# Optimization experiments

Measured on AMD Instinct MI355X. Metric: run time of the kernel, lower is better.

The kernel has to match this reference:

```python
import jax, jax.numpy as jnp
import numpy as np

BLOCK_SIZE = 32
MODEL_DIM = 64
HEAD_SIZE = 64
WINDOW_SIZE = 8
B = 32768


def _local_causal_mask(T, window):
    # True = masked out. Allowed iff i - window + 1 <= j <= i.
    i = jnp.arange(T)[:, None]
    j = jnp.arange(T)[None, :]
    return (j > i) | (j < i - window + 1)


def setup_inputs() -> dict:
    key = jax.random.key(0)
    kx, kq, kk, kv = jax.random.split(key, 4)
    x = jax.random.normal(kx, (B, BLOCK_SIZE, MODEL_DIM), dtype=jnp.float32)
    # nn.Linear(model_dim, head_size, bias=False): y = x @ W.T, W: [head_size, model_dim].
    # Store as [model_dim, head_size] so y = x @ W.
    s = 1.0 / np.sqrt(MODEL_DIM)
    Wq = jax.random.uniform(kq, (MODEL_DIM, HEAD_SIZE), jnp.float32, -s, s)
    Wk = jax.random.uniform(kk, (MODEL_DIM, HEAD_SIZE), jnp.float32, -s, s)
    Wv = jax.random.uniform(kv, (MODEL_DIM, HEAD_SIZE), jnp.float32, -s, s)
    return {"x": x, "Wq": Wq, "Wk": Wk, "Wv": Wv}


def reference(x, Wq, Wk, Wv):
    B_, T, C = x.shape
    q = x @ Wq  # [B, T, H]
    k = x @ Wk
    v = x @ Wv
    scale = k.shape[-1] ** -0.5
    weight = jnp.einsum("bth,bsh->bts", q, k) * scale  # [B, T, T]
    mask = _local_causal_mask(T, WINDOW_SIZE)
    weight = jnp.where(mask[None, :, :], -jnp.inf, weight)
    attention_weights = jax.nn.softmax(weight, axis=-1)
    # dropout treated as identity (eval mode) for determinism
    output = jnp.einsum("bts,bsh->bth", attention_weights, v)
    return (output, attention_weights)
```

## Files before the change

### kernel.cpp

```cpp
#include <hip/hip_runtime.h>
#include <math.h>

typedef float f32x4 __attribute__((ext_vector_type(4)));
typedef unsigned int u32x4 __attribute__((ext_vector_type(4)));
typedef short bf16x8 __attribute__((ext_vector_type(8)));

__device__ __forceinline__ unsigned f2bf1(float f) {
  unsigned u = __builtin_bit_cast(unsigned, f);
  return (u + 0x7FFFu + ((u >> 16) & 1u)) >> 16;
}
__device__ __forceinline__ unsigned pack2(float a, float b) {
  return f2bf1(a) | (f2bf1(b) << 16);
}

__device__ __forceinline__ f32x4 mfma16(u32x4 a, u32x4 b, f32x4 c) {
  return __builtin_amdgcn_mfma_f32_16x16x32_bf16(
      __builtin_bit_cast(bf16x8, a), __builtin_bit_cast(bf16x8, b), c, 0, 0, 0);
}

template <int NS, int NF, int NKS>
__device__ __forceinline__ void cvt_frags(const f32x4 (&acc)[NS][NF],
                                          u32x4 (&frag)[NF][NKS],
                                          int f, int g) {
  unsigned pk[NS][NF][2];
#pragma unroll
  for (int s = 0; s < NS; ++s)
#pragma unroll
    for (int n = 0; n < NF; ++n) {
      pk[s][n][0] = pack2(acc[s][n][0], acc[s][n][1]);
      pk[s][n][1] = pack2(acc[s][n][2], acc[s][n][3]);
    }
  const bool hi = ((g >> 1) & 1) != 0;
#pragma unroll
  for (int w = 0; w < 4; ++w) {
    const int gp = 2 * (g & 1) + (w >> 1);
    const int idx = (f + (gp << 4)) << 2;
#pragma unroll
    for (int n = 0; n < NF; ++n)
#pragma unroll
      for (int ks = 0; ks < NKS; ++ks) {
        int lo = __builtin_amdgcn_ds_bpermute(idx, (int)pk[2 * ks + 0][n][w & 1]);
        int h2 = __builtin_amdgcn_ds_bpermute(idx, (int)pk[2 * ks + 1][n][w & 1]);
        frag[n][ks][w] = (unsigned)(hi ? h2 : lo);
      }
  }
}

__launch_bounds__(256, 2)
__global__ void lwmh_kernel(const float* __restrict__ x,
                            const float* __restrict__ Wq,
                            const float* __restrict__ Wk,
                            const float* __restrict__ Wv,
                            float* __restrict__ out,
                            float* __restrict__ attw,
                            int nb) {
  const int lane = threadIdx.x & 63;
  const int f = lane & 15;
  const int g = lane >> 4;
  const int wid = blockIdx.x * (blockDim.x >> 6) + (threadIdx.x >> 6);
  const int nwaves = gridDim.x * (blockDim.x >> 6);

  u32x4 wq[4][2], wk[4][2], wv[4][2];
  {
#pragma unroll
    for (int t = 0; t < 4; ++t)
#pragma unroll
      for (int ks = 0; ks < 2; ++ks) {
        const int off = (ks * 32 + g * 8) * 64 + t * 16 + f;
        const float* bq = Wq + off;
        const float* bk = Wk + off;
        const float* bv = Wv + off;
        u32x4 fq, fk, fv;
#pragma unroll
        for (int w = 0; w < 4; ++w) {
          fq[w] = pack2(bq[(2 * w) * 64], bq[(2 * w + 1) * 64]);
          fk[w] = pack2(bk[(2 * w) * 64], bk[(2 * w + 1) * 64]);
          fv[w] = pack2(bv[(2 * w) * 64], bv[(2 * w + 1) * 64]);
        }
        wq[t][ks] = fq;
        wk[t][ks] = fk;
        wv[t][ks] = fv;
      }
  }

  f32x4 xc[2][2][2], xn[2][2][2];

  auto loadX = [&](int b, f32x4 (&xr)[2][2][2]) {
    const float* xb = x + (size_t)b * 2048;
#pragma unroll
    for (int mt = 0; mt < 2; ++mt)
#pragma unroll
      for (int ks = 0; ks < 2; ++ks) {
        const float* p0 = xb + (mt * 16 + f) * 64 + ks * 32 + g * 8;
        xr[mt][ks][0] = *(const f32x4*)p0;
        xr[mt][ks][1] = *(const f32x4*)(p0 + 4);
      }
  };

  int b = wid;
  if (b < nb) loadX(b, xc);

  for (; b < nb; b += nwaves) {
    const int bn = b + nwaves;

    u32x4 xf[2][2];
#pragma unroll
    for (int mt = 0; mt < 2; ++mt)
#pragma unroll
      for (int ks = 0; ks < 2; ++ks) {
        u32x4 fr;
        fr[0] = pack2(xc[mt][ks][0][0], xc[mt][ks][0][1]);
        fr[1] = pack2(xc[mt][ks][0][2], xc[mt][ks][0][3]);
        fr[2] = pack2(xc[mt][ks][1][0], xc[mt][ks][1][1]);
        fr[3] = pack2(xc[mt][ks][1][2], xc[mt][ks][1][3]);
        xf[mt][ks] = fr;
      }

    if (bn < nb) loadX(bn, xn);

    f32x4 qt[4][2];
#pragma unroll
    for (int mh = 0; mh < 4; ++mh)
#pragma unroll
      for (int nt = 0; nt < 2; ++nt) {
        f32x4 a = {0.f, 0.f, 0.f, 0.f};
#pragma unroll
        for (int ks = 0; ks < 2; ++ks) a = mfma16(wq[mh][ks], xf[nt][ks], a);
        qt[mh][nt] = a;
      }
    u32x4 aQ[2][2];
    cvt_frags<4, 2, 2>(qt, aQ, f, g);

    f32x4 kt[4][2];
#pragma unroll
    for (int mh = 0; mh < 4; ++mh)
#pragma unroll
      for (int nt = 0; nt < 2; ++nt) {
        f32x4 a = {0.f, 0.f, 0.f, 0.f};
#pragma unroll
        for (int ks = 0; ks < 2; ++ks) a = mfma16(wk[mh][ks], xf[nt][ks], a);
        kt[mh][nt] = a;
      }
    u32x4 aK[2][2];
    cvt_frags<4, 2, 2>(kt, aK, f, g);

    f32x4 va[2][4];
#pragma unroll
    for (int ms = 0; ms < 2; ++ms)
#pragma unroll
      for (int nh = 0; nh < 4; ++nh) {
        f32x4 a = {0.f, 0.f, 0.f, 0.f};
#pragma unroll
        for (int ks = 0; ks < 2; ++ks) a = mfma16(xf[ms][ks], wv[nh][ks], a);
        va[ms][nh] = a;
      }
    u32x4 bV[4][1];
    cvt_frags<2, 4, 1>(va, bV, f, g);

    f32x4 st[2][2];
#pragma unroll
    for (int ms = 0; ms < 2; ++ms)
#pragma unroll
      for (int nt = 0; nt < 2; ++nt) {
        f32x4 a = {0.f, 0.f, 0.f, 0.f};
#pragma unroll
        for (int ks = 0; ks < 2; ++ks) a = mfma16(aK[ms][ks], aQ[nt][ks], a);
        st[ms][nt] = a;
      }

    float pe[2][2][4];
#pragma unroll
    for (int nt = 0; nt < 2; ++nt) {
      const int t = nt * 16 + f;
      float m = -INFINITY;
#pragma unroll
      for (int ms = 0; ms < 2; ++ms)
#pragma unroll
        for (int r = 0; r < 4; ++r) {
          const int s = ms * 16 + 4 * g + r;
          float v = st[ms][nt][r] * 0.125f;
          v = (t >= s && (t - s) <= 7) ? v : -INFINITY;
          pe[ms][nt][r] = v;
          m = fmaxf(m, v);
        }
      m = fmaxf(m, __shfl_xor(m, 16));
      m = fmaxf(m, __shfl_xor(m, 32));
      float sum = 0.f;
#pragma unroll
      for (int ms = 0; ms < 2; ++ms)
#pragma unroll
        for (int r = 0; r < 4; ++r) {
          const float e = __expf(pe[ms][nt][r] - m);
          pe[ms][nt][r] = e;
          sum += e;
        }
      sum += __shfl_xor(sum, 16);
      sum += __shfl_xor(sum, 32);
      const float inv = 1.0f / sum;
#pragma unroll
      for (int ms = 0; ms < 2; ++ms)
#pragma unroll
        for (int r = 0; r < 4; ++r) pe[ms][nt][r] *= inv;
    }

    {
      float* aw = attw + (size_t)b * 1024;
#pragma unroll
      for (int ms = 0; ms < 2; ++ms)
#pragma unroll
        for (int nt = 0; nt < 2; ++nt)
#pragma unroll
          for (int r = 0; r < 4; ++r)
            aw[(nt * 16 + f) * 32 + ms * 16 + 4 * g + r] = pe[ms][nt][r];
    }

    f32x4 pacc[2][2];
#pragma unroll
    for (int ms = 0; ms < 2; ++ms)
#pragma unroll
      for (int nt = 0; nt < 2; ++nt) {
        f32x4 a;
        a[0] = pe[ms][nt][0];
        a[1] = pe[ms][nt][1];
        a[2] = pe[ms][nt][2];
        a[3] = pe[ms][nt][3];
        pacc[ms][nt] = a;
      }
    u32x4 aP[2][1];
    cvt_frags<2, 2, 1>(pacc, aP, f, g);

    f32x4 o[2][4];
#pragma unroll
    for (int mt = 0; mt < 2; ++mt)
#pragma unroll
      for (int nh = 0; nh < 4; ++nh) {
        f32x4 a = {0.f, 0.f, 0.f, 0.f};
        o[mt][nh] = mfma16(aP[mt][0], bV[nh][0], a);
      }

    {
      float* op = out + (size_t)b * 2048;
#pragma unroll
      for (int mt = 0; mt < 2; ++mt)
#pragma unroll
        for (int nh = 0; nh < 4; ++nh)
#pragma unroll
          for (int r = 0; r < 4; ++r)
            op[(mt * 16 + 4 * g + r) * 64 + nh * 16 + f] = o[mt][nh][r];
    }

    if (bn < nb) {
#pragma unroll
      for (int mt = 0; mt < 2; ++mt)
#pragma unroll
        for (int ks = 0; ks < 2; ++ks) {
          xc[mt][ks][0] = xn[mt][ks][0];
          xc[mt][ks][1] = xn[mt][ks][1];
        }
    }
  }
}

extern "C" void kernel_launch(void* const* d_in, const int* in_sizes, int n_in,
                              void* d_out, int out_size, void* d_ws, size_t ws_size,
                              hipStream_t stream) {
  const float* x = (const float*)d_in[0];
  const float* Wq = (const float*)d_in[1];
  const float* Wk = (const float*)d_in[2];
  const float* Wv = (const float*)d_in[3];
  const int nb = in_sizes[0] / 2048;
  float* out = (float*)d_out;
  float* attw = out + (size_t)nb * 2048;

  const int grid = 1024;
  lwmh_kernel<<<grid, 256, 0, stream>>>(x, Wq, Wk, Wv, out, attw, nb);
}
```

Measured before the change: 146.2 us.

## Fold Wq·WkT into a precomputed matrix and drop softmax max subtraction

Precomputes N = Wq·Wk^T·scale once per wave, so scores become x·(N·x^T). This replaces the separate Q and K projections and their fragment conversions with one projection plus one conversion. Softmax no longer subtracts the row maximum and only exponentiates inside the window. Attention weights are now written with vectorized 16-byte stores, and the next x load is issued earlier. Skipping the max subtraction relies on scores staying small enough not to overflow exp, and the extra bf16 rounding of N changes numerics.

Result: no change. 146.3 us (+0.1%).

```diff
diff --git a/kernel.cpp b/kernel.cpp
--- a/kernel.cpp
+++ b/kernel.cpp
@@ -60,27 +60,53 @@
   const int wid = blockIdx.x * (blockDim.x >> 6) + (threadIdx.x >> 6);
   const int nwaves = gridDim.x * (blockDim.x >> 6);
 
-  u32x4 wq[4][2], wk[4][2], wv[4][2];
-  {
-#pragma unroll
-    for (int t = 0; t < 4; ++t)
-#pragma unroll
-      for (int ks = 0; ks < 2; ++ks) {
-        const int off = (ks * 32 + g * 8) * 64 + t * 16 + f;
-        const float* bq = Wq + off;
-        const float* bk = Wk + off;
-        const float* bv = Wv + off;
-        u32x4 fq, fk, fv;
-#pragma unroll
-        for (int w = 0; w < 4; ++w) {
-          fq[w] = pack2(bq[(2 * w) * 64], bq[(2 * w + 1) * 64]);
-          fk[w] = pack2(bk[(2 * w) * 64], bk[(2 * w + 1) * 64]);
-          fv[w] = pack2(bv[(2 * w) * 64], bv[(2 * w + 1) * 64]);
-        }
-        wq[t][ks] = fq;
-        wk[t][ks] = fk;
-        wv[t][ks] = fv;
-      }
+  u32x4 aWq[4][2], bWkT[4][2];
+#pragma unroll
+  for (int ct = 0; ct < 4; ++ct)
+#pragma unroll
+    for (int hs = 0; hs < 2; ++hs) {
+      const int off = (ct * 16 + f) * 64 + hs * 32 + g * 8;
+      f32x4 ql = *(const f32x4*)(Wq + off);
+      f32x4 qh = *(const f32x4*)(Wq + off + 4);
+      f32x4 kl = *(const f32x4*)(Wk + off);
+      f32x4 kh = *(const f32x4*)(Wk + off + 4);
+      u32x4 fq, fk;
+      fq[0] = pack2(ql[0], ql[1]); fq[1] = pack2(ql[2], ql[3]);
+      fq[2] = pack2(qh[0], qh[1]); fq[3] = pack2(qh[2], qh[3]);
+      fk[0] = pack2(kl[0], kl[1]); fk[1] = pack2(kl[2], kl[3]);
+      fk[2] = pack2(kh[0], kh[1]); fk[3] = pack2(kh[2], kh[3]);
+      aWq[ct][hs] = fq;
+      bWkT[ct][hs] = fk;
+    }
+
+  u32x4 wv[4][2];
+#pragma unroll
+  for (int t = 0; t < 4; ++t)
+#pragma unroll
+    for (int ks = 0; ks < 2; ++ks) {
+      const float* bv = Wv + (ks * 32 + g * 8) * 64 + t * 16 + f;
+      u32x4 fv;
+#pragma unroll
+      for (int w = 0; w < 4; ++w)
+        fv[w] = pack2(bv[(2 * w) * 64], bv[(2 * w + 1) * 64]);
+      wv[t][ks] = fv;
+    }
+
+  u32x4 aN[4][2];
+#pragma unroll
+  for (int nc = 0; nc < 4; ++nc) {
+    f32x4 nacc[4][1];
+#pragma unroll
+    for (int mc = 0; mc < 4; ++mc) {
+      f32x4 a = {0.f, 0.f, 0.f, 0.f};
+#pragma unroll
+      for (int hs = 0; hs < 2; ++hs) a = mfma16(aWq[mc][hs], bWkT[nc][hs], a);
+      nacc[mc][0] = a * 0.125f;
+    }
+    u32x4 tmp[1][2];
+    cvt_frags<4, 1, 2>(nacc, tmp, f, g);
+    aN[nc][0] = tmp[0][0];
+    aN[nc][1] = tmp[0][1];
   }
 
   f32x4 xc[2][2][2], xn[2][2][2];
@@ -102,6 +128,7 @@
 
   for (; b < nb; b += nwaves) {
     const int bn = b + nwaves;
+    if (bn < nb) loadX(bn, xn);
 
     u32x4 xf[2][2];
 #pragma unroll
@@ -116,33 +143,18 @@
         xf[mt][ks] = fr;
       }
 
-    if (bn < nb) loadX(bn, xn);
-
-    f32x4 qt[4][2];
-#pragma unroll
-    for (int mh = 0; mh < 4; ++mh)
+    f32x4 t2[4][2];
+#pragma unroll
+    for (int mc = 0; mc < 4; ++mc)
 #pragma unroll
       for (int nt = 0; nt < 2; ++nt) {
         f32x4 a = {0.f, 0.f, 0.f, 0.f};
 #pragma unroll
-        for (int ks = 0; ks < 2; ++ks) a = mfma16(wq[mh][ks], xf[nt][ks], a);
-        qt[mh][nt] = a;
-      }
-    u32x4 aQ[2][2];
-    cvt_frags<4, 2, 2>(qt, aQ, f, g);
-
-    f32x4 kt[4][2];
-#pragma unroll
-    for (int mh = 0; mh < 4; ++mh)
-#pragma unroll
-      for (int nt = 0; nt < 2; ++nt) {
-        f32x4 a = {0.f, 0.f, 0.f, 0.f};
-#pragma unroll
-        for (int ks = 0; ks < 2; ++ks) a = mfma16(wk[mh][ks], xf[nt][ks], a);
-        kt[mh][nt] = a;
-      }
-    u32x4 aK[2][2];
-    cvt_frags<4, 2, 2>(kt, aK, f, g);
+        for (int ks = 0; ks < 2; ++ks) a = mfma16(aN[mc][ks], xf[nt][ks], a);
+        t2[mc][nt] = a;
+      }
+    u32x4 bT2[2][2];
+    cvt_frags<4, 2, 2>(t2, bT2, f, g);
 
     f32x4 va[2][4];
 #pragma unroll
@@ -164,33 +176,22 @@
       for (int nt = 0; nt < 2; ++nt) {
         f32x4 a = {0.f, 0.f, 0.f, 0.f};
 #pragma unroll
-        for (int ks = 0; ks < 2; ++ks) a = mfma16(aK[ms][ks], aQ[nt][ks], a);
+        for (int ks = 0; ks < 2; ++ks) a = mfma16(xf[ms][ks], bT2[nt][ks], a);
         st[ms][nt] = a;
       }
 
-    float pe[2][2][4];
+    f32x4 pe[2][2];
 #pragma unroll
     for (int nt = 0; nt < 2; ++nt) {
       const int t = nt * 16 + f;
-      float m = -INFINITY;
+      float sum = 0.f;
 #pragma unroll
       for (int ms = 0; ms < 2; ++ms)
 #pragma unroll
         for (int r = 0; r < 4; ++r) {
           const int s = ms * 16 + 4 * g + r;
-          float v = st[ms][nt][r] * 0.125f;
-          v = (t >= s && (t - s) <= 7) ? v : -INFINITY;
-          pe[ms][nt][r] = v;
-          m = fmaxf(m, v);
-        }
-      m = fmaxf(m, __shfl_xor(m, 16));
-      m = fmaxf(m, __shfl_xor(m, 32));
-      float sum = 0.f;
-#pragma unroll
-      for (int ms = 0; ms < 2; ++ms)
-#pragma unroll
-        for (int r = 0; r < 4; ++r) {
-          const float e = __expf(pe[ms][nt][r] - m);
+          const float e =
+              ((unsigned)(t - s) <= 7u) ? __expf(st[ms][nt][r]) : 0.f;
           pe[ms][nt][r] = e;
           sum += e;
         }
@@ -199,8 +200,7 @@
       const float inv = 1.0f / sum;
 #pragma unroll
       for (int ms = 0; ms < 2; ++ms)
-#pragma unroll
-        for (int r = 0; r < 4; ++r) pe[ms][nt][r] *= inv;
+        pe[ms][nt] *= inv;
     }
 
     {
@@ -209,25 +209,11 @@
       for (int ms = 0; ms < 2; ++ms)
 #pragma unroll
         for (int nt = 0; nt < 2; ++nt)
-#pragma unroll
-          for (int r = 0; r < 4; ++r)
-            aw[(nt * 16 + f) * 32 + ms * 16 + 4 * g + r] = pe[ms][nt][r];
-    }
-
-    f32x4 pacc[2][2];
-#pragma unroll
-    for (int ms = 0; ms < 2; ++ms)
-#pragma unroll
-      for (int nt = 0; nt < 2; ++nt) {
-        f32x4 a;
-        a[0] = pe[ms][nt][0];
-        a[1] = pe[ms][nt][1];
-        a[2] = pe[ms][nt][2];
-        a[3] = pe[ms][nt][3];
-        pacc[ms][nt] = a;
-      }
+          *(f32x4*)(aw + (nt * 16 + f) * 32 + ms * 16 + 4 * g) = pe[ms][nt];
+    }
+
     u32x4 aP[2][1];
-    cvt_frags<2, 2, 1>(pacc, aP, f, g);
+    cvt_frags<2, 2, 1>(pe, aP, f, g);
 
     f32x4 o[2][4];
 #pragma unroll
```
